# Kernel tuning notes

Hardware: AMD Instinct MI355X
Metric: run time of the kernel (lower is better)

The kernel has to match this reference:

```python
import jax, jax.numpy as jnp
import numpy as np

H = 32          # query heads
D = 128         # head_dim
THETA = 10000.0
NEG = -1e30


def _rope_cos_sin(positions, d):
    half = d // 2
    inv_freq = 1.0 / (THETA ** (jnp.arange(0, d, 2, dtype=jnp.float32) / d))  # [half]
    ang = positions.astype(jnp.float32)[:, None] * inv_freq[None, :]          # [B, half]
    return jnp.cos(ang), jnp.sin(ang)


def _apply_rope(x, cos, sin):
    # neox-style rotary on last dim; cos/sin broadcast over leading dims
    half = x.shape[-1] // 2
    x1, x2 = x[..., :half], x[..., half:]
    return jnp.concatenate([x1 * cos - x2 * sin, x2 * cos + x1 * sin], axis=-1)


def setup_inputs() -> dict:
    key = jax.random.key(0)
    ks = jax.random.split(key, 8)
    B, hidden = 64, 4096
    num_blocks, block_size, max_blocks = 16384, 16, 256
    hidden_states = jax.random.normal(ks[0], (B, hidden), dtype=jnp.float32)
    wqkv = jax.random.normal(ks[1], (hidden, (H + 2) * D), dtype=jnp.float32) * 0.02
    wdense = jax.random.normal(ks[2], (hidden, hidden), dtype=jnp.float32) * 0.02
    k_cache = jax.random.normal(ks[3], (num_blocks, block_size, D), dtype=jnp.float32)
    v_cache = jax.random.normal(ks[4], (num_blocks, block_size, D), dtype=jnp.float32)
    # each sequence owns a distinct set of 256 blocks
    block_tables = jnp.arange(B * max_blocks, dtype=jnp.int64).reshape(B, max_blocks)
    context_lens = jax.random.randint(ks[5], (B,), 1, max_blocks * block_size + 1).astype(jnp.int64)
    positions = context_lens - 1  # position of the new (current) token
    return {
        "hidden_states": hidden_states, "wqkv": wqkv, "wdense": wdense,
        "k_cache": k_cache, "v_cache": v_cache,
        "positions": positions, "block_tables": block_tables,
        "context_lens": context_lens,
    }


def reference(hidden_states, wqkv, wdense, k_cache, v_cache,
              positions, block_tables, context_lens):
    B = hidden_states.shape[0]
    block_size = k_cache.shape[1]
    scale = 1.0 / np.sqrt(D).astype(np.float32)

    # fused QKV projection (bias=False in Falcon-7B config)
    qkv = hidden_states @ wqkv                                  # [B,(H+2)*D]
    q = qkv[:, : H * D].reshape(B, H, D)
    k = qkv[:, H * D : (H + 1) * D]                             # [B,D]  (MQA, 1 kv head)
    v = qkv[:, (H + 1) * D :]                                   # [B,D]

    # rotary embedding on q and k at the current positions
    cos, sin = _rope_cos_sin(positions, D)                      # [B,D/2]
    q = _apply_rope(q, cos[:, None, :], sin[:, None, :])
    k = _apply_rope(k, cos, sin)

    # write the new token's k/v into the paged cache (scatter)
    rows = jnp.arange(B)
    blk = block_tables[rows, positions // block_size]           # [B]
    off = positions % block_size
    k_cache = k_cache.at[blk, off].set(k)
    v_cache = v_cache.at[blk, off].set(v)

    # paged gather: assemble each sequence's KV from its block table
    keys = k_cache[block_tables].reshape(B, -1, D)              # [B,L,D]
    vals = v_cache[block_tables].reshape(B, -1, D)
    L = keys.shape[1]

    scores = jnp.einsum('bhd,bld->bhl', q, keys) * scale        # [B,H,L]
    valid = jnp.arange(L)[None, :] < context_lens[:, None]      # [B,L]
    scores = jnp.where(valid[:, None, :], scores, NEG)
    probs = jax.nn.softmax(scores, axis=-1)
    attn = jnp.einsum('bhl,bld->bhd', probs, vals).reshape(B, H * D)

    return attn @ wdense                                        # [B,hidden]
```

## Files before the change

kernel.cpp:

```cpp
#include <hip/hip_runtime.h>
#include <hip/hip_bf16.h>
#include <cmath>

#define NHEADS 32
#define DIM 128
#define SPLITS 16
#define TILE 32
#define KSPLIT 8
#define QKV_N 4352
#define HID 4096

typedef __attribute__((ext_vector_type(4))) float f32x4;
typedef __attribute__((ext_vector_type(8))) short short8i;
typedef __attribute__((ext_vector_type(4))) short short4i;

__device__ __forceinline__ unsigned short f2bf(float x) {
  __hip_bfloat16 h = __float2bfloat16(x);
  return *reinterpret_cast<unsigned short*>(&h);
}
__device__ __forceinline__ unsigned int pk2bf(float lo, float hi) {
  return (unsigned)f2bf(lo) | ((unsigned)f2bf(hi) << 16);
}
__device__ __forceinline__ float bf2f(unsigned short u) {
  unsigned int b = ((unsigned int)u) << 16;
  return __uint_as_float(b);
}

__device__ __forceinline__ f32x4 mfma16bf16(short4i a, short4i b, f32x4 c) {
#if __has_builtin(__builtin_amdgcn_mfma_f32_16x16x16bf16_1k)
  return __builtin_amdgcn_mfma_f32_16x16x16bf16_1k(a, b, c, 0, 0, 0);
#else
  asm volatile("v_mfma_f32_16x16x16_bf16 %0, %1, %2, %0"
               : "+v"(c) : "v"(a), "v"(b));
  return c;
#endif
}

__global__ __launch_bounds__(256, 4) void gemm64_mfma(
    const float* __restrict__ A, const float* __restrict__ W,
    float* __restrict__ P, int N, int K)
{
  __shared__ unsigned short Ab[64][40];
  __shared__ unsigned short Wt[64][40];
  const int t = threadIdx.x;
  const int w = t >> 6, lane = t & 63;
  const int l4 = lane >> 4, l16 = lane & 15;
  const int n0 = blockIdx.x * 64;
  const int KS = K / KSPLIT;
  const int kbase = blockIdx.y * KS;

  const int ar = t >> 2, akq = t & 3;
  const int bn = t & 63, bkq = t >> 6;

  f32x4 acc[4];
#pragma unroll
  for (int i = 0; i < 4; ++i) acc[i] = (f32x4){0.f, 0.f, 0.f, 0.f};

  float4 a0, a1;
  float bw[8];

#define GLOAD(KC)                                                          \
  {                                                                        \
    const float* ap = A + (size_t)ar * K + kbase + (KC) + akq * 8;         \
    a0 = *(const float4*)ap;                                               \
    a1 = *(const float4*)(ap + 4);                                         \
    const float* wp = W + (size_t)(kbase + (KC) + bkq * 8) * N + n0 + bn;  \
    _Pragma("unroll")                                                      \
    for (int j = 0; j < 8; ++j) bw[j] = wp[(size_t)j * N];                 \
  }

#define SWRITE                                                             \
  {                                                                        \
    unsigned int ua[4] = {pk2bf(a0.x, a0.y), pk2bf(a0.z, a0.w),            \
                          pk2bf(a1.x, a1.y), pk2bf(a1.z, a1.w)};           \
    *(float4*)&Ab[ar][akq * 8] = *(float4*)ua;                             \
    unsigned int ub[4] = {pk2bf(bw[0], bw[1]), pk2bf(bw[2], bw[3]),        \
                          pk2bf(bw[4], bw[5]), pk2bf(bw[6], bw[7])};       \
    *(float4*)&Wt[bn][bkq * 8] = *(float4*)ub;                             \
  }

  GLOAD(0);
  SWRITE;
  __syncthreads();

  for (int kc = 0; kc < KS; kc += 32) {
    const bool pre = (kc + 32 < KS);
    if (pre) GLOAD(kc + 32);

    const short8i af = *(const short8i*)&Ab[w * 16 + l16][l4 * 8];
#pragma unroll
    for (int nt = 0; nt < 4; ++nt) {
      const short8i bf = *(const short8i*)&Wt[nt * 16 + l16][l4 * 8];
      acc[nt] = __builtin_amdgcn_mfma_f32_16x16x32_bf16(af, bf, acc[nt], 0, 0, 0);
    }

    __syncthreads();
    if (pre) {
      SWRITE;
      __syncthreads();
    }
  }

  float* base = P + (size_t)blockIdx.y * 64 * N + n0;
#pragma unroll
  for (int nt = 0; nt < 4; ++nt)
#pragma unroll
    for (int r = 0; r < 4; ++r)
      base[(size_t)(w * 16 + l4 * 4 + r) * N + nt * 16 + l16] = acc[nt][r];
#undef GLOAD
#undef SWRITE
}

__global__ __launch_bounds__(256) void reduce_parts(
    const float* __restrict__ P, float* __restrict__ C, int total)
{
  const int i = (blockIdx.x * 256 + threadIdx.x) * 4;
  if (i >= total) return;
  float4 s = *(const float4*)(P + i);
#pragma unroll
  for (int k = 1; k < KSPLIT; ++k) {
    const float4 v = *(const float4*)(P + (size_t)k * total + i);
    s.x += v.x; s.y += v.y; s.z += v.z; s.w += v.w;
  }
  *(float4*)(C + i) = s;
}

__global__ __launch_bounds__(256) void reduce_rope(
    const float* __restrict__ P, float* __restrict__ qkv,
    const int* __restrict__ positions)
{
  const int id = blockIdx.x * 256 + threadIdx.x;
  const int b = id / 560;
  const int w = id - b * 560;
  const int total = 64 * QKV_N;
  const size_t rbase = (size_t)b * QKV_N;

  if (w < 528) {
    const int r = w >> 4;
    const int g = w & 15;
    const int base = (r < 32) ? r * DIM : HID;
    const int c1 = base + g * 4;
    const int c2 = c1 + 64;
    float4 s1 = *(const float4*)(P + rbase + c1);
    float4 s2 = *(const float4*)(P + rbase + c2);
#pragma unroll
    for (int k = 1; k < KSPLIT; ++k) {
      const float4 v1 = *(const float4*)(P + (size_t)k * total + rbase + c1);
      const float4 v2 = *(const float4*)(P + (size_t)k * total + rbase + c2);
      s1.x += v1.x; s1.y += v1.y; s1.z += v1.z; s1.w += v1.w;
      s2.x += v2.x; s2.y += v2.y; s2.z += v2.z; s2.w += v2.w;
    }
    const float pos = (float)positions[b];
    float o1[4], o2[4];
    const float sv1[4] = {s1.x, s1.y, s1.z, s1.w};
    const float sv2[4] = {s2.x, s2.y, s2.z, s2.w};
#pragma unroll
    for (int j = 0; j < 4; ++j) {
      const int d = g * 4 + j;
      const float ex = (float)d * (1.0f / 64.0f);
      const float inv = 1.0f / powf(10000.0f, ex);
      const float ang = pos * inv;
      const float c = cosf(ang), sn = sinf(ang);
      o1[j] = sv1[j] * c - sv2[j] * sn;
      o2[j] = sv2[j] * c + sv1[j] * sn;
    }
    *(float4*)(qkv + rbase + c1) = make_float4(o1[0], o1[1], o1[2], o1[3]);
    *(float4*)(qkv + rbase + c2) = make_float4(o2[0], o2[1], o2[2], o2[3]);
  } else {
    const int c = HID + DIM + (w - 528) * 4;
    float4 s = *(const float4*)(P + rbase + c);
#pragma unroll
    for (int k = 1; k < KSPLIT; ++k) {
      const float4 v = *(const float4*)(P + (size_t)k * total + rbase + c);
      s.x += v.x; s.y += v.y; s.z += v.z; s.w += v.w;
    }
    *(float4*)(qkv + rbase + c) = s;
  }
}

__global__ __launch_bounds__(256, 4) void attn_kernel(
    const float* __restrict__ qkv,
    const float* __restrict__ k_cache, const float* __restrict__ v_cache,
    const int* __restrict__ block_tables, const int* __restrict__ context_lens,
    float* __restrict__ pl, unsigned short* __restrict__ pacc)
{
  const int b = blockIdx.x, s = blockIdx.y;
  const int t = threadIdx.x;
  const int w = t >> 6, lane = t & 63;
  const int hq = w >> 1, pq = w & 1;
  const int l4 = lane >> 4, l16 = lane & 15;
  const int ctx = context_lens[b];
  const int pos = ctx - 1;
  const int chunk = (ctx + SPLITS - 1) / SPLITS;
  const int start = s * chunk;
  const int end = min(start + chunk, ctx);
  const int nt = (end > start) ? ((end - start + TILE - 1) / TILE) : 0;

  __shared__ unsigned short KbU[32 * 128];
  __shared__ unsigned short VtU[128 * 34];
  __shared__ int bt_lds[24];

  const float* qbase = qkv + (size_t)b * QKV_N;
  const int bt0 = start >> 4;
  if (t < 24) {
    const int idx = bt0 + t;
    bt_lds[t] = (idx < 256) ? block_tables[b * 256 + idx] : 0;
  }

  const float scale = 0.08838834764831845f;
  short8i qf[4];
  {
    const float* qp0 = qbase + (hq * 16 + l16) * DIM + l4 * 8;
#pragma unroll
    for (int ks = 0; ks < 4; ++ks) {
      const float4 a = *(const float4*)(qp0 + ks * 32);
      const float4 c = *(const float4*)(qp0 + ks * 32 + 4);
      union { unsigned int u[4]; short8i v; } qc;
      qc.u[0] = pk2bf(a.x * scale, a.y * scale);
      qc.u[1] = pk2bf(a.z * scale, a.w * scale);
      qc.u[2] = pk2bf(c.x * scale, c.y * scale);
      qc.u[3] = pk2bf(c.z * scale, c.w * scale);
      qf[ks] = qc.v;
    }
  }

  f32x4 o2[8];
#pragma unroll
  for (int i = 0; i < 8; ++i) o2[i] = (f32x4){0.f, 0.f, 0.f, 0.f};
  float lh = 0.f;

  float4 kreg[4], vreg[4];
  const int tk_sub = t >> 5;
  const int tk_col = t & 31;
  const int vp2 = tk_sub + 8 * (tk_col >> 4);
  const int vd0 = (tk_col & 15) * 8;

#define LOADREGS(T0)                                                     \
  {                                                                      \
    _Pragma("unroll")                                                    \
    for (int j = 0; j < 4; ++j) {                                        \
      int gp_ = (T0) + j * 8 + tk_sub;                                   \
      if (gp_ > pos) gp_ = pos;                                          \
      const float* kp;                                                   \
      if (gp_ == pos) kp = qbase + HID;                                  \
      else {                                                             \
        const int blk = bt_lds[(gp_ >> 4) - bt0];                        \
        kp = k_cache + ((size_t)blk * 16 + (gp_ & 15)) * DIM;            \
      }                                                                  \
      kreg[j] = *(const float4*)(kp + tk_col * 4);                       \
    }                                                                    \
    _Pragma("unroll")                                                    \
    for (int j = 0; j < 2; ++j) {                                        \
      int gv_ = (T0) + vp2 * 2 + j;                                      \
      if (gv_ > pos) gv_ = pos;                                          \
      const float* vp;                                                   \
      if (gv_ == pos) vp = qbase + HID + DIM;                            \
      else {                                                             \
        const int blk = bt_lds[(gv_ >> 4) - bt0];                        \
        vp = v_cache + ((size_t)blk * 16 + (gv_ & 15)) * DIM;            \
      }                                                                  \
      vreg[j * 2 + 0] = *(const float4*)(vp + vd0);                      \
      vreg[j * 2 + 1] = *(const float4*)(vp + vd0 + 4);                  \
    }                                                                    \
  }

#define WRITE_TILE                                                                     \
  {                                                                                    \
    _Pragma("unroll")                                                                  \
    for (int j = 0; j < 4; ++j) {                                                      \
      const int pl_ = j * 8 + tk_sub;                                                  \
      const int up = (tk_col >> 1) ^ (pl_ & 15);                                       \
      unsigned int* kd = (unsigned int*)&KbU[pl_ * 128 + up * 8 + (tk_col & 1) * 4];   \
      kd[0] = pk2bf(kreg[j].x, kreg[j].y);                                             \
      kd[1] = pk2bf(kreg[j].z, kreg[j].w);                                             \
    }                                                                                  \
    {                                                                                  \
      const int pc_ = vp2 * 2;                                                         \
      *(unsigned int*)&VtU[(vd0 + 0) * 34 + pc_] = pk2bf(vreg[0].x, vreg[2].x);        \
      *(unsigned int*)&VtU[(vd0 + 1) * 34 + pc_] = pk2bf(vreg[0].y, vreg[2].y);        \
      *(unsigned int*)&VtU[(vd0 + 2) * 34 + pc_] = pk2bf(vreg[0].z, vreg[2].z);        \
      *(unsigned int*)&VtU[(vd0 + 3) * 34 + pc_] = pk2bf(vreg[0].w, vreg[2].w);        \
      *(unsigned int*)&VtU[(vd0 + 4) * 34 + pc_] = pk2bf(vreg[1].x, vreg[3].x);        \
      *(unsigned int*)&VtU[(vd0 + 5) * 34 + pc_] = pk2bf(vreg[1].y, vreg[3].y);        \
      *(unsigned int*)&VtU[(vd0 + 6) * 34 + pc_] = pk2bf(vreg[1].z, vreg[3].z);        \
      *(unsigned int*)&VtU[(vd0 + 7) * 34 + pc_] = pk2bf(vreg[1].w, vreg[3].w);        \
    }                                                                                  \
  }

  if (nt > 0) {
    __syncthreads();
    LOADREGS(start);
    WRITE_TILE;
    __syncthreads();

    for (int it = 0; it < nt; ++it) {
      const int t0 = start + it * TILE;
      const bool pre = (it + 1 < nt);
      if (pre) LOADREGS(t0 + TILE);

      f32x4 accs = {0.f, 0.f, 0.f, 0.f};
      const int rowK = pq * 16 + l16;
#pragma unroll
      for (int ks = 0; ks < 4; ++ks) {
        const int up = (l4 + ks * 4) ^ l16;
        const short8i kf = *(const short8i*)&KbU[rowK * 128 + up * 8];
        accs = __builtin_amdgcn_mfma_f32_16x16x32_bf16(kf, qf[ks], accs, 0, 0, 0);
      }

      const int pb_ = t0 + pq * 16 + l4 * 4;
      const float p0 = (pb_ + 0 < end) ? __expf(accs[0]) : 0.f;
      const float p1 = (pb_ + 1 < end) ? __expf(accs[1]) : 0.f;
      const float p2 = (pb_ + 2 < end) ? __expf(accs[2]) : 0.f;
      const float p3 = (pb_ + 3 < end) ? __expf(accs[3]) : 0.f;
      lh += (p0 + p1) + (p2 + p3);
      union { unsigned int u[2]; short4i v; } pc;
      pc.u[0] = pk2bf(p0, p1);
      pc.u[1] = pk2bf(p2, p3);
      const short4i pf = pc.v;

      const int vb = pq * 16 + l4 * 4;
#pragma unroll
      for (int ob = 0; ob < 8; ++ob) {
        const int rowV = ob * 16 + l16;
        union { unsigned int u[2]; short4i v; } vc;
        vc.u[0] = *(const unsigned int*)&VtU[rowV * 34 + vb];
        vc.u[1] = *(const unsigned int*)&VtU[rowV * 34 + vb + 2];
        o2[ob] = mfma16bf16(pf, vc.v, o2[ob]);
      }

      if (pre) {
        __syncthreads();
        WRITE_TILE;
        __syncthreads();
      }
    }
  }

  float lhr = lh;
  lhr += __shfl_xor(lhr, 16);
  lhr += __shfl_xor(lhr, 32);

  const size_t slot = ((size_t)(b * SPLITS + s) * 2 + pq) * NHEADS + hq * 16;
#pragma unroll
  for (int ob = 0; ob < 8; ++ob) {
    pacc[(slot + l4 * 4 + 0) * DIM + ob * 16 + l16] = f2bf(o2[ob][0]);
    pacc[(slot + l4 * 4 + 1) * DIM + ob * 16 + l16] = f2bf(o2[ob][1]);
    pacc[(slot + l4 * 4 + 2) * DIM + ob * 16 + l16] = f2bf(o2[ob][2]);
    pacc[(slot + l4 * 4 + 3) * DIM + ob * 16 + l16] = f2bf(o2[ob][3]);
  }
  if (lane < 16) pl[slot + lane] = lhr;
#undef LOADREGS
#undef WRITE_TILE
}

__global__ __launch_bounds__(128) void combine_kernel(
    const float* __restrict__ pl, const unsigned short* __restrict__ pacc,
    float* __restrict__ attn)
{
  const int bh = blockIdx.x;
  const int b = bh >> 5, h = bh & 31;
  const int d = threadIdx.x;
  float L = 0.f, o = 0.f;
#pragma unroll 4
  for (int j = 0; j < SPLITS * 2; ++j) {
    const size_t idx = ((size_t)b * SPLITS * 2 + j) * NHEADS + h;
    L += pl[idx];
    o += bf2f(pacc[idx * DIM + d]);
  }
  attn[(size_t)b * HID + h * DIM + d] = o / L;
}

extern "C" void kernel_launch(void* const* d_in, const int* in_sizes, int n_in,
                              void* d_out, int out_size, void* d_ws, size_t ws_size,
                              hipStream_t stream) {
  const float* hidden   = (const float*)d_in[0];
  const float* wqkv     = (const float*)d_in[1];
  const float* wdense   = (const float*)d_in[2];
  const float* k_cache  = (const float*)d_in[3];
  const float* v_cache  = (const float*)d_in[4];
  const int* positions    = (const int*)d_in[5];
  const int* block_tables = (const int*)d_in[6];
  const int* context_lens = (const int*)d_in[7];
  float* out = (float*)d_out;

  float* qkv  = (float*)d_ws;
  float* attn = qkv + 64 * QKV_N;
  float* un   = attn + 64 * HID;
  float* gp   = un;
  unsigned short* pacc = (unsigned short*)un;
  float* pl   = un + (size_t)64 * SPLITS * 2 * NHEADS * DIM / 2;

  gemm64_mfma<<<dim3(QKV_N / 64, KSPLIT), 256, 0, stream>>>(hidden, wqkv, gp, QKV_N, HID);
  reduce_rope<<<140, 256, 0, stream>>>(gp, qkv, positions);
  attn_kernel<<<dim3(64, SPLITS), 256, 0, stream>>>(qkv, k_cache, v_cache,
                                                    block_tables, context_lens, pl, pacc);
  combine_kernel<<<64 * NHEADS, 128, 0, stream>>>(pl, pacc, attn);
  gemm64_mfma<<<dim3(HID / 64, KSPLIT), 256, 0, stream>>>(attn, wdense, gp, HID, HID);
  reduce_parts<<<(64 * HID) / 1024, 256, 0, stream>>>(gp, out, 64 * HID);
}
```

Measured before the change: 92.46 us.

## Deepen KV prefetch to two tiles ahead with packed bf16 staging registers

The attention loop now keeps two tiles of K/V in flight: the next tile is already converted to packed bf16 registers while the one after is loaded from global memory. The goal is to hide more global-load latency behind the MFMA work of the current tile. In exchange it uses more registers (16 extra u32), which may lower occupancy. It also adds an unconditional barrier on the last iteration.

```diff
diff --git a/kernel.cpp b/kernel.cpp
--- a/kernel.cpp
+++ b/kernel.cpp
@@ -230,6 +230,7 @@
   float lh = 0.f;
 
   float4 kreg[4], vreg[4];
+  unsigned int ku[8], vu[8];
   const int tk_sub = t >> 5;
   const int tk_col = t & 31;
   const int vp2 = tk_sub + 8 * (tk_col >> 4);
@@ -264,39 +265,55 @@
     }                                                                    \
   }
 
-#define WRITE_TILE                                                                     \
-  {                                                                                    \
-    _Pragma("unroll")                                                                  \
-    for (int j = 0; j < 4; ++j) {                                                      \
-      const int pl_ = j * 8 + tk_sub;                                                  \
-      const int up = (tk_col >> 1) ^ (pl_ & 15);                                       \
-      unsigned int* kd = (unsigned int*)&KbU[pl_ * 128 + up * 8 + (tk_col & 1) * 4];   \
-      kd[0] = pk2bf(kreg[j].x, kreg[j].y);                                             \
-      kd[1] = pk2bf(kreg[j].z, kreg[j].w);                                             \
-    }                                                                                  \
-    {                                                                                  \
-      const int pc_ = vp2 * 2;                                                         \
-      *(unsigned int*)&VtU[(vd0 + 0) * 34 + pc_] = pk2bf(vreg[0].x, vreg[2].x);        \
-      *(unsigned int*)&VtU[(vd0 + 1) * 34 + pc_] = pk2bf(vreg[0].y, vreg[2].y);        \
-      *(unsigned int*)&VtU[(vd0 + 2) * 34 + pc_] = pk2bf(vreg[0].z, vreg[2].z);        \
-      *(unsigned int*)&VtU[(vd0 + 3) * 34 + pc_] = pk2bf(vreg[0].w, vreg[2].w);        \
-      *(unsigned int*)&VtU[(vd0 + 4) * 34 + pc_] = pk2bf(vreg[1].x, vreg[3].x);        \
-      *(unsigned int*)&VtU[(vd0 + 5) * 34 + pc_] = pk2bf(vreg[1].y, vreg[3].y);        \
-      *(unsigned int*)&VtU[(vd0 + 6) * 34 + pc_] = pk2bf(vreg[1].z, vreg[3].z);        \
-      *(unsigned int*)&VtU[(vd0 + 7) * 34 + pc_] = pk2bf(vreg[1].w, vreg[3].w);        \
-    }                                                                                  \
+#define CVT_TILE                                                         \
+  {                                                                      \
+    _Pragma("unroll")                                                    \
+    for (int j = 0; j < 4; ++j) {                                        \
+      ku[j * 2 + 0] = pk2bf(kreg[j].x, kreg[j].y);                       \
+      ku[j * 2 + 1] = pk2bf(kreg[j].z, kreg[j].w);                       \
+    }                                                                    \
+    vu[0] = pk2bf(vreg[0].x, vreg[2].x);                                 \
+    vu[1] = pk2bf(vreg[0].y, vreg[2].y);                                 \
+    vu[2] = pk2bf(vreg[0].z, vreg[2].z);                                 \
+    vu[3] = pk2bf(vreg[0].w, vreg[2].w);                                 \
+    vu[4] = pk2bf(vreg[1].x, vreg[3].x);                                 \
+    vu[5] = pk2bf(vreg[1].y, vreg[3].y);                                 \
+    vu[6] = pk2bf(vreg[1].z, vreg[3].z);                                 \
+    vu[7] = pk2bf(vreg[1].w, vreg[3].w);                                 \
+  }
+
+#define WRITE_TILE                                                                   \
+  {                                                                                  \
+    _Pragma("unroll")                                                                \
+    for (int j = 0; j < 4; ++j) {                                                    \
+      const int pl_ = j * 8 + tk_sub;                                                \
+      const int up = (tk_col >> 1) ^ (pl_ & 15);                                     \
+      unsigned int* kd = (unsigned int*)&KbU[pl_ * 128 + up * 8 + (tk_col & 1) * 4]; \
+      kd[0] = ku[j * 2 + 0];                                                         \
+      kd[1] = ku[j * 2 + 1];                                                         \
+    }                                                                                \
+    {                                                                                \
+      const int pc_ = vp2 * 2;                                                       \
+      _Pragma("unroll")                                                              \
+      for (int d = 0; d < 8; ++d)                                                    \
+        *(unsigned int*)&VtU[(vd0 + d) * 34 + pc_] = vu[d];                          \
+    }                                                                                \
   }
 
   if (nt > 0) {
     __syncthreads();
     LOADREGS(start);
+    CVT_TILE;
+    if (nt > 1) LOADREGS(start + TILE);
     WRITE_TILE;
     __syncthreads();
 
     for (int it = 0; it < nt; ++it) {
       const int t0 = start + it * TILE;
-      const bool pre = (it + 1 < nt);
-      if (pre) LOADREGS(t0 + TILE);
+      const bool h1 = (it + 1 < nt);
+      const bool h2 = (it + 2 < nt);
+      if (h1) CVT_TILE;
+      if (h2) LOADREGS(t0 + 2 * TILE);
 
       f32x4 accs = {0.f, 0.f, 0.f, 0.f};
       const int rowK = pq * 16 + l16;
@@ -328,8 +345,8 @@
         o2[ob] = mfma16bf16(pf, vc.v, o2[ob]);
       }
 
-      if (pre) {
-        __syncthreads();
+      __syncthreads();
+      if (h1) {
         WRITE_TILE;
         __syncthreads();
       }
@@ -350,6 +367,7 @@
   }
   if (lane < 16) pl[slot + lane] = lhr;
 #undef LOADREGS
+#undef CVT_TILE
 #undef WRITE_TILE
 }
 
```

Result: slower. 96.15 us (+4.0%).

## Split attention into single-wave blocks loading K directly into registers

Applied to the files above, without the earlier changes.

Each attention workgroup becomes one 64-lane wave, and the four waves per (batch, split) move onto a third grid dimension. The shared K tile, the block-wide barriers and the register prefetch of the next tile all go away. Each wave now loads its 16 K rows straight into MFMA operand registers and stages its own 16-position V slice through a smaller per-wave LDS buffer. The goal is to remove barrier stalls and LDS traffic for K. The cost is that waves for different head groups now fetch the same K/V rows twice, and there is no longer any overlap of the next tile's loads with compute.

```diff
diff --git a/kernel.cpp b/kernel.cpp
--- a/kernel.cpp
+++ b/kernel.cpp
@@ -178,16 +178,16 @@
   }
 }
 
-__global__ __launch_bounds__(256, 4) void attn_kernel(
+#define VSTRU 18
+__global__ __launch_bounds__(64, 3) void attn_kernel(
     const float* __restrict__ qkv,
     const float* __restrict__ k_cache, const float* __restrict__ v_cache,
     const int* __restrict__ block_tables, const int* __restrict__ context_lens,
     float* __restrict__ pl, unsigned short* __restrict__ pacc)
 {
-  const int b = blockIdx.x, s = blockIdx.y;
-  const int t = threadIdx.x;
-  const int w = t >> 6, lane = t & 63;
+  const int b = blockIdx.x, s = blockIdx.y, w = blockIdx.z;
   const int hq = w >> 1, pq = w & 1;
+  const int lane = threadIdx.x;
   const int l4 = lane >> 4, l16 = lane & 15;
   const int ctx = context_lens[b];
   const int pos = ctx - 1;
@@ -196,15 +196,14 @@
   const int end = min(start + chunk, ctx);
   const int nt = (end > start) ? ((end - start + TILE - 1) / TILE) : 0;
 
-  __shared__ unsigned short KbU[32 * 128];
-  __shared__ unsigned short VtU[128 * 34];
+  __shared__ unsigned short VtU[128 * VSTRU];
   __shared__ int bt_lds[24];
 
   const float* qbase = qkv + (size_t)b * QKV_N;
   const int bt0 = start >> 4;
-  if (t < 24) {
-    const int idx = bt0 + t;
-    bt_lds[t] = (idx < 256) ? block_tables[b * 256 + idx] : 0;
+  if (lane < 24) {
+    const int idx = bt0 + lane;
+    bt_lds[lane] = (idx < 256) ? block_tables[b * 256 + idx] : 0;
   }
 
   const float scale = 0.08838834764831845f;
@@ -229,110 +228,88 @@
   for (int i = 0; i < 8; ++i) o2[i] = (f32x4){0.f, 0.f, 0.f, 0.f};
   float lh = 0.f;
 
-  float4 kreg[4], vreg[4];
-  const int tk_sub = t >> 5;
-  const int tk_col = t & 31;
-  const int vp2 = tk_sub + 8 * (tk_col >> 4);
-  const int vd0 = (tk_col & 15) * 8;
-
-#define LOADREGS(T0)                                                     \
-  {                                                                      \
-    _Pragma("unroll")                                                    \
-    for (int j = 0; j < 4; ++j) {                                        \
-      int gp_ = (T0) + j * 8 + tk_sub;                                   \
-      if (gp_ > pos) gp_ = pos;                                          \
-      const float* kp;                                                   \
-      if (gp_ == pos) kp = qbase + HID;                                  \
-      else {                                                             \
-        const int blk = bt_lds[(gp_ >> 4) - bt0];                        \
-        kp = k_cache + ((size_t)blk * 16 + (gp_ & 15)) * DIM;            \
-      }                                                                  \
-      kreg[j] = *(const float4*)(kp + tk_col * 4);                       \
-    }                                                                    \
-    _Pragma("unroll")                                                    \
-    for (int j = 0; j < 2; ++j) {                                        \
-      int gv_ = (T0) + vp2 * 2 + j;                                      \
-      if (gv_ > pos) gv_ = pos;                                          \
-      const float* vp;                                                   \
-      if (gv_ == pos) vp = qbase + HID + DIM;                            \
-      else {                                                             \
-        const int blk = bt_lds[(gv_ >> 4) - bt0];                        \
-        vp = v_cache + ((size_t)blk * 16 + (gv_ & 15)) * DIM;            \
-      }                                                                  \
-      vreg[j * 2 + 0] = *(const float4*)(vp + vd0);                      \
-      vreg[j * 2 + 1] = *(const float4*)(vp + vd0 + 4);                  \
-    }                                                                    \
-  }
-
-#define WRITE_TILE                                                                     \
-  {                                                                                    \
-    _Pragma("unroll")                                                                  \
-    for (int j = 0; j < 4; ++j) {                                                      \
-      const int pl_ = j * 8 + tk_sub;                                                  \
-      const int up = (tk_col >> 1) ^ (pl_ & 15);                                       \
-      unsigned int* kd = (unsigned int*)&KbU[pl_ * 128 + up * 8 + (tk_col & 1) * 4];   \
-      kd[0] = pk2bf(kreg[j].x, kreg[j].y);                                             \
-      kd[1] = pk2bf(kreg[j].z, kreg[j].w);                                             \
-    }                                                                                  \
-    {                                                                                  \
-      const int pc_ = vp2 * 2;                                                         \
-      *(unsigned int*)&VtU[(vd0 + 0) * 34 + pc_] = pk2bf(vreg[0].x, vreg[2].x);        \
-      *(unsigned int*)&VtU[(vd0 + 1) * 34 + pc_] = pk2bf(vreg[0].y, vreg[2].y);        \
-      *(unsigned int*)&VtU[(vd0 + 2) * 34 + pc_] = pk2bf(vreg[0].z, vreg[2].z);        \
-      *(unsigned int*)&VtU[(vd0 + 3) * 34 + pc_] = pk2bf(vreg[0].w, vreg[2].w);        \
-      *(unsigned int*)&VtU[(vd0 + 4) * 34 + pc_] = pk2bf(vreg[1].x, vreg[3].x);        \
-      *(unsigned int*)&VtU[(vd0 + 5) * 34 + pc_] = pk2bf(vreg[1].y, vreg[3].y);        \
-      *(unsigned int*)&VtU[(vd0 + 6) * 34 + pc_] = pk2bf(vreg[1].z, vreg[3].z);        \
-      *(unsigned int*)&VtU[(vd0 + 7) * 34 + pc_] = pk2bf(vreg[1].w, vreg[3].w);        \
-    }                                                                                  \
-  }
-
-  if (nt > 0) {
-    __syncthreads();
-    LOADREGS(start);
-    WRITE_TILE;
-    __syncthreads();
-
-    for (int it = 0; it < nt; ++it) {
-      const int t0 = start + it * TILE;
-      const bool pre = (it + 1 < nt);
-      if (pre) LOADREGS(t0 + TILE);
-
-      f32x4 accs = {0.f, 0.f, 0.f, 0.f};
-      const int rowK = pq * 16 + l16;
-#pragma unroll
-      for (int ks = 0; ks < 4; ++ks) {
-        const int up = (l4 + ks * 4) ^ l16;
-        const short8i kf = *(const short8i*)&KbU[rowK * 128 + up * 8];
-        accs = __builtin_amdgcn_mfma_f32_16x16x32_bf16(kf, qf[ks], accs, 0, 0, 0);
+  const int vp2 = lane >> 3;
+  const int vd0 = (lane & 7) * 16;
+
+  for (int it = 0; it < nt; ++it) {
+    const int t0 = start + it * TILE + pq * 16;
+
+    int kr = t0 + l16;
+    if (kr > pos) kr = pos;
+    const float* kp;
+    if (kr == pos) kp = qbase + HID;
+    else {
+      const int blk = bt_lds[(kr >> 4) - bt0];
+      kp = k_cache + ((size_t)blk * 16 + (kr & 15)) * DIM;
+    }
+    float4 kraw[8];
+#pragma unroll
+    for (int ks = 0; ks < 4; ++ks) {
+      kraw[ks * 2 + 0] = *(const float4*)(kp + ks * 32 + l4 * 8);
+      kraw[ks * 2 + 1] = *(const float4*)(kp + ks * 32 + l4 * 8 + 4);
+    }
+
+    int r0 = t0 + 2 * vp2, r1 = r0 + 1;
+    if (r0 > pos) r0 = pos;
+    if (r1 > pos) r1 = pos;
+    const float* vpt0;
+    const float* vpt1;
+    if (r0 == pos) vpt0 = qbase + HID + DIM;
+    else {
+      const int blk = bt_lds[(r0 >> 4) - bt0];
+      vpt0 = v_cache + ((size_t)blk * 16 + (r0 & 15)) * DIM;
+    }
+    if (r1 == pos) vpt1 = qbase + HID + DIM;
+    else {
+      const int blk = bt_lds[(r1 >> 4) - bt0];
+      vpt1 = v_cache + ((size_t)blk * 16 + (r1 & 15)) * DIM;
+    }
+    float4 vraw[8];
+#pragma unroll
+    for (int j = 0; j < 4; ++j) {
+      vraw[j]     = *(const float4*)(vpt0 + vd0 + j * 4);
+      vraw[4 + j] = *(const float4*)(vpt1 + vd0 + j * 4);
+    }
+
+    f32x4 accs = {0.f, 0.f, 0.f, 0.f};
+#pragma unroll
+    for (int ks = 0; ks < 4; ++ks) {
+      union { unsigned int u[4]; short8i v; } kc;
+      kc.u[0] = pk2bf(kraw[ks * 2].x,     kraw[ks * 2].y);
+      kc.u[1] = pk2bf(kraw[ks * 2].z,     kraw[ks * 2].w);
+      kc.u[2] = pk2bf(kraw[ks * 2 + 1].x, kraw[ks * 2 + 1].y);
+      kc.u[3] = pk2bf(kraw[ks * 2 + 1].z, kraw[ks * 2 + 1].w);
+      accs = __builtin_amdgcn_mfma_f32_16x16x32_bf16(kc.v, qf[ks], accs, 0, 0, 0);
+    }
+
+    {
+      const float* v0 = (const float*)vraw;
+      const float* v1 = (const float*)(vraw + 4);
+#pragma unroll
+      for (int dd = 0; dd < 16; ++dd) {
+        const int od = vd0 + dd;
+        *(unsigned int*)&VtU[od * VSTRU + vp2 * 2] = pk2bf(v0[dd], v1[dd]);
       }
-
-      const int pb_ = t0 + pq * 16 + l4 * 4;
-      const float p0 = (pb_ + 0 < end) ? __expf(accs[0]) : 0.f;
-      const float p1 = (pb_ + 1 < end) ? __expf(accs[1]) : 0.f;
-      const float p2 = (pb_ + 2 < end) ? __expf(accs[2]) : 0.f;
-      const float p3 = (pb_ + 3 < end) ? __expf(accs[3]) : 0.f;
-      lh += (p0 + p1) + (p2 + p3);
-      union { unsigned int u[2]; short4i v; } pc;
-      pc.u[0] = pk2bf(p0, p1);
-      pc.u[1] = pk2bf(p2, p3);
-      const short4i pf = pc.v;
-
-      const int vb = pq * 16 + l4 * 4;
-#pragma unroll
-      for (int ob = 0; ob < 8; ++ob) {
-        const int rowV = ob * 16 + l16;
-        union { unsigned int u[2]; short4i v; } vc;
-        vc.u[0] = *(const unsigned int*)&VtU[rowV * 34 + vb];
-        vc.u[1] = *(const unsigned int*)&VtU[rowV * 34 + vb + 2];
-        o2[ob] = mfma16bf16(pf, vc.v, o2[ob]);
-      }
-
-      if (pre) {
-        __syncthreads();
-        WRITE_TILE;
-        __syncthreads();
-      }
+    }
+
+    const int pb_ = t0 + l4 * 4;
+    const float p0 = (pb_ + 0 < end) ? __expf(accs[0]) : 0.f;
+    const float p1 = (pb_ + 1 < end) ? __expf(accs[1]) : 0.f;
+    const float p2 = (pb_ + 2 < end) ? __expf(accs[2]) : 0.f;
+    const float p3 = (pb_ + 3 < end) ? __expf(accs[3]) : 0.f;
+    lh += (p0 + p1) + (p2 + p3);
+    union { unsigned int u[2]; short4i v; } pc;
+    pc.u[0] = pk2bf(p0, p1);
+    pc.u[1] = pk2bf(p2, p3);
+    const short4i pf = pc.v;
+
+#pragma unroll
+    for (int ob = 0; ob < 8; ++ob) {
+      const int rowV = ob * 16 + l16;
+      union { unsigned int u[2]; short4i v; } vc;
+      vc.u[0] = *(const unsigned int*)&VtU[rowV * VSTRU + l4 * 4];
+      vc.u[1] = *(const unsigned int*)&VtU[rowV * VSTRU + l4 * 4 + 2];
+      o2[ob] = mfma16bf16(pf, vc.v, o2[ob]);
     }
   }
 
@@ -349,8 +326,6 @@
     pacc[(slot + l4 * 4 + 3) * DIM + ob * 16 + l16] = f2bf(o2[ob][3]);
   }
   if (lane < 16) pl[slot + lane] = lhr;
-#undef LOADREGS
-#undef WRITE_TILE
 }
 
 __global__ __launch_bounds__(128) void combine_kernel(
@@ -392,8 +367,8 @@
 
   gemm64_mfma<<<dim3(QKV_N / 64, KSPLIT), 256, 0, stream>>>(hidden, wqkv, gp, QKV_N, HID);
   reduce_rope<<<140, 256, 0, stream>>>(gp, qkv, positions);
-  attn_kernel<<<dim3(64, SPLITS), 256, 0, stream>>>(qkv, k_cache, v_cache,
-                                                    block_tables, context_lens, pl, pacc);
+  attn_kernel<<<dim3(64, SPLITS, 4), 64, 0, stream>>>(qkv, k_cache, v_cache,
+                                                      block_tables, context_lens, pl, pacc);
   combine_kernel<<<64 * NHEADS, 128, 0, stream>>>(pl, pacc, attn);
   gemm64_mfma<<<dim3(HID / 64, KSPLIT), 256, 0, stream>>>(attn, wdense, gp, HID, HID);
   reduce_parts<<<(64 * HID) / 1024, 256, 0, stream>>>(gp, out, 64 * HID);
```

After: 122.8 us. +32.8%, slower.
